# Kernel optimization log

Measured on AMD Instinct MI355X. Metric: run time of the kernel, lower is better.

The kernel has to match this reference:

```python
import jax, jax.numpy as jnp
import numpy as np

B, L, C, H, W = 2, 16, 16, 64, 64


def setup_inputs() -> dict:
    key = jax.random.key(0)
    k1, k2 = jax.random.split(key)
    # flows scaled so cumulative normalized-coordinate flows mostly stay in [-1, 1]
    flows = jax.random.normal(k1, (B, L, 2, H, W), dtype=jnp.float32) * 0.05
    images = jax.random.normal(k2, (B, L, C, H, W), dtype=jnp.float32)
    return {"flows": flows, "images": images}


def _bilinear_sample(images, gx, gy):
    # images: [B, Lj, C, H, W]; gx, gy: [B, Li, Lj, H, W] normalized coords in [-1, 1]
    # Replicates torch.nn.functional.grid_sample(mode='bilinear',
    # padding_mode='zeros', align_corners=False).
    Bs, Lj, Cs, Hs, Ws = images.shape
    ix = ((gx + 1.0) * Ws - 1.0) * 0.5  # pixel x coord
    iy = ((gy + 1.0) * Hs - 1.0) * 0.5  # pixel y coord
    x0f = jnp.floor(ix)
    y0f = jnp.floor(iy)
    wx = ix - x0f  # weight toward x0+1 (differentiable w.r.t. flow)
    wy = iy - y0f
    x0 = x0f.astype(jnp.int32)
    y0 = y0f.astype(jnp.int32)
    img_flat = images.reshape(Bs, Lj, Cs, Hs * Ws)

    def gather(xi, yi):
        valid = (xi >= 0) & (xi < Ws) & (yi >= 0) & (yi < Hs)  # [B,Li,Lj,H,W]
        lin = jnp.clip(yi, 0, Hs - 1) * Ws + jnp.clip(xi, 0, Ws - 1)
        lin_t = jnp.transpose(lin, (0, 2, 1, 3, 4))  # [B,Lj,Li,H,W]
        # per (b, j): gather [C, HW] at indices [Li, H, W] -> [C, Li, H, W]
        v = jax.vmap(jax.vmap(lambda im, l: im[:, l]))(img_flat, lin_t)
        v = jnp.transpose(v, (0, 3, 1, 2, 4, 5))  # [B,Li,Lj,C,H,W]
        return v * valid[:, :, :, None, :, :].astype(v.dtype)

    v00 = gather(x0, y0)
    v01 = gather(x0 + 1, y0)
    v10 = gather(x0, y0 + 1)
    v11 = gather(x0 + 1, y0 + 1)
    wX = wx[:, :, :, None, :, :]
    wY = wy[:, :, :, None, :, :]
    return (v00 * (1.0 - wX) * (1.0 - wY) + v01 * wX * (1.0 - wY)
            + v10 * (1.0 - wX) * wY + v11 * wX * wY)


def reference(flows, images):
    Bs, Ls, _, Hs, Ws = flows.shape
    dt = flows.dtype
    cum = jnp.cumsum(flows, axis=1)  # [B,L,2,H,W]
    # rel[b, i, j] = cum[b, i] - cum[b, j]  -> [B,Li,Lj,2,H,W]
    rel = cum[:, :, None] - cum[:, None, :]
    # base sampling grid (pixel centers in normalized coords)
    gx_base = (jnp.arange(Ws, dtype=dt) + 0.5) * (2.0 / Ws) - 1.0  # [W]
    gy_base = (jnp.arange(Hs, dtype=dt) + 0.5) * (2.0 / Hs) - 1.0  # [H]
    gx = gx_base + rel[:, :, :, 0]              # [B,Li,Lj,H,W]
    gy = gy_base[:, None] + rel[:, :, :, 1]     # [B,Li,Lj,H,W]
    gx = jnp.remainder(gx + 1.0, 2.0) - 1.0     # wrap x into [-1, 1)
    warped = _bilinear_sample(images, gx, gy)   # [B,Li,Lj,C,H,W]
    mask = jnp.tril(jnp.ones((Ls, Ls), dtype=dt))
    # causal accumulate over source index j
    return jnp.einsum('bijchw,ij->bichw', warped, mask)
```

## Files before the change

kernel.cpp:

```cpp
#include <hip/hip_runtime.h>

#define BB 2
#define LL 16
#define CC 16
#define HH 64
#define WW 64
#define HWSZ (HH * WW)
#define NSEG 36

__device__ __constant__ int SEG_I[NSEG] = {
    1, 2, 3, 4,
    5, 5, 6, 6, 7, 7, 8, 8,
    9, 9, 9, 10, 10, 10, 11, 11, 11, 12, 12, 12,
    13, 13, 13, 13, 14, 14, 14, 14, 15, 15, 15, 15};
__device__ __constant__ int SEG_J0[NSEG] = {
    0, 0, 0, 0,
    0, 4, 0, 4, 0, 4, 0, 4,
    0, 4, 8, 0, 4, 8, 0, 4, 8, 0, 4, 8,
    0, 4, 8, 12, 0, 4, 8, 12, 0, 4, 8, 12};

__device__ __constant__ signed char NSEG_OF_I[LL] = {0,1,1,1,1,2,2,2,2,3,3,3,3,4,4,4};
__device__ __constant__ signed char SEG_OF_I[LL][4] = {
    {0,0,0,0},
    {0,0,0,0}, {1,0,0,0}, {2,0,0,0}, {3,0,0,0},
    {4,5,0,0}, {6,7,0,0}, {8,9,0,0}, {10,11,0,0},
    {12,13,14,0}, {15,16,17,0}, {18,19,20,0}, {21,22,23,0},
    {24,25,26,27}, {28,29,30,31}, {32,33,34,35}};

#define CUM2_FLOATS (BB * LL * HWSZ * 2)
#define QP_FLOATS   (BB * LL * CC * HWSZ)

__global__ __launch_bounds__(256) void gsp_prep(
    const float* __restrict__ flows,
    const float* __restrict__ images,
    float2* __restrict__ cum2,
    float4* __restrict__ nhwc)
{
    if (blockIdx.x < 32) {
        const int gid = blockIdx.x * 256 + threadIdx.x;
        const int b   = gid >> 12;
        const int pix = gid & (HWSZ - 1);
        const float* fb = flows + (size_t)b * LL * 2 * HWSZ + pix;
        float vx[LL], vy[LL];
        #pragma unroll
        for (int l = 0; l < LL; ++l) {
            vx[l] = fb[(size_t)l * 2 * HWSZ];
            vy[l] = fb[(size_t)l * 2 * HWSZ + HWSZ];
        }
        #pragma unroll
        for (int l = 1; l < LL; ++l) { vx[l] += vx[l - 1]; vy[l] += vy[l - 1]; }
        float2* cb = cum2 + (size_t)b * LL * HWSZ + pix;
        #pragma unroll
        for (int l = 0; l < LL; ++l) {
            float2 v; v.x = vx[l]; v.y = vy[l];
            cb[(size_t)l * HWSZ] = v;
        }
    } else {
        const int gid  = (blockIdx.x - 32) * 256 + threadIdx.x;
        const int quad = gid & 3;
        const int pix  = (gid >> 2) & (HWSZ - 1);
        const int bl   = gid >> 14;

        const float* src = images + (size_t)(bl * CC + quad * 4) * HWSZ + pix;
        float4 v;
        v.x = src[0 * HWSZ];
        v.y = src[1 * HWSZ];
        v.z = src[2 * HWSZ];
        v.w = src[3 * HWSZ];
        nhwc[((size_t)bl * HWSZ + pix) * 4 + quad] = v;
    }
}

__global__ __launch_bounds__(256) void gsp_pairs(
    const float2* __restrict__ cum2,
    const float4* __restrict__ nhwc,
    float4* __restrict__ partial)
{
    const int tile = blockIdx.x & 63;
    const int seg  = (blockIdx.x >> 6) % NSEG;
    const int b    = blockIdx.x / (64 * NSEG);

    const int i    = SEG_I[seg];
    const int j0   = SEG_J0[seg];
    const int jmax = i - 1;

    const int psub = threadIdx.x >> 2;
    const int quad = threadIdx.x & 3;
    const int pix  = tile * 64 + psub;
    const int h = pix >> 6;
    const int w = pix & (WW - 1);

    const float2* cum_b  = cum2 + (size_t)b * LL * HWSZ + pix;
    const float4* nhwc_b = nhwc + (size_t)b * LL * HWSZ * 4;

    const float gxb = (w + 0.5f) * (2.0f / WW) - 1.0f;
    const float gyb = (h + 0.5f) * (2.0f / HH) - 1.0f;

    const float2 ci = cum_b[(size_t)i * HWSZ];
    int    jj[4];
    float2 cj[4];
    #pragma unroll
    for (int k = 0; k < 4; ++k) {
        jj[k] = min(j0 + k, jmax);
        cj[k] = cum_b[(size_t)jj[k] * HWSZ];
    }

    int   off[16];
    float fxk[4], fyk[4];
    float m00[4], m01[4], m10[4], m11[4];
    #pragma unroll
    for (int k = 0; k < 4; ++k) {
        float gx = gxb + (ci.x - cj[k].x);
        float gy = gyb + (ci.y - cj[k].y);

        float tt = gx + 1.0f;
        tt = tt - floorf(tt * 0.5f) * 2.0f;
        gx = tt - 1.0f;

        const float ix = ((gx + 1.0f) * WW - 1.0f) * 0.5f;
        const float iy = ((gy + 1.0f) * HH - 1.0f) * 0.5f;
        const float x0f = floorf(ix);
        const float y0f = floorf(iy);
        fxk[k] = ix - x0f;
        fyk[k] = iy - y0f;
        const int x0 = (int)x0f;
        const int y0 = (int)y0f;
        const int x1 = x0 + 1;
        const int y1 = y0 + 1;

        const bool vx0 = (x0 >= 0) && (x0 < WW);
        const bool vx1 = (x1 >= 0) && (x1 < WW);
        const bool vy0 = (y0 >= 0) && (y0 < HH);
        const bool vy1 = (y1 >= 0) && (y1 < HH);
        const float wpad = (j0 + k <= jmax) ? 1.0f : 0.0f;
        m00[k] = (vx0 && vy0) ? wpad : 0.0f;
        m01[k] = (vx1 && vy0) ? wpad : 0.0f;
        m10[k] = (vx0 && vy1) ? wpad : 0.0f;
        m11[k] = (vx1 && vy1) ? wpad : 0.0f;

        const int cx0 = min(max(x0, 0), WW - 1);
        const int cx1 = min(max(x1, 0), WW - 1);
        const int cy0 = min(max(y0, 0), HH - 1);
        const int cy1 = min(max(y1, 0), HH - 1);

        const int jbase = jj[k] * (HWSZ * 4) + quad;
        off[k * 4 + 0] = jbase + (cy0 * WW + cx0) * 4;
        off[k * 4 + 1] = jbase + (cy0 * WW + cx1) * 4;
        off[k * 4 + 2] = jbase + (cy1 * WW + cx0) * 4;
        off[k * 4 + 3] = jbase + (cy1 * WW + cx1) * 4;
    }

    float4 v[16];
    #pragma unroll
    for (int m = 0; m < 16; ++m) v[m] = nhwc_b[off[m]];

    float wgt[16];
    #pragma unroll
    for (int k = 0; k < 4; ++k) {
        const float fx = fxk[k], fy = fyk[k];
        wgt[k * 4 + 0] = m00[k] * (1.0f - fx) * (1.0f - fy);
        wgt[k * 4 + 1] = m01[k] * fx * (1.0f - fy);
        wgt[k * 4 + 2] = m10[k] * (1.0f - fx) * fy;
        wgt[k * 4 + 3] = m11[k] * fx * fy;
    }

    float4 s; s.x = 0.0f; s.y = 0.0f; s.z = 0.0f; s.w = 0.0f;
    #pragma unroll
    for (int m = 0; m < 16; ++m) {
        s.x += wgt[m] * v[m].x;
        s.y += wgt[m] * v[m].y;
        s.z += wgt[m] * v[m].z;
        s.w += wgt[m] * v[m].w;
    }
    partial[((size_t)(b * NSEG + seg) * HWSZ + pix) * 4 + quad] = s;
}

__global__ __launch_bounds__(256) void gsp_reduce(
    const float4* __restrict__ nhwc,
    const float4* __restrict__ partial,
    float* __restrict__ out)
{
    const int gid  = blockIdx.x * 256 + threadIdx.x;
    const int quad = gid & 3;
    const int pix  = (gid >> 2) & (HWSZ - 1);
    const int bl   = gid >> 14;
    const int b    = bl >> 4;
    const int i    = bl & 15;

    float4 s = nhwc[((size_t)bl * HWSZ + pix) * 4 + quad];

    const int n = NSEG_OF_I[i];
    for (int k = 0; k < n; ++k) {
        const int seg = SEG_OF_I[i][k];
        const float4 p = partial[((size_t)(b * NSEG + seg) * HWSZ + pix) * 4 + quad];
        s.x += p.x; s.y += p.y; s.z += p.z; s.w += p.w;
    }

    float* op = out + ((size_t)bl * CC + quad * 4) * HWSZ + pix;
    op[0 * HWSZ] = s.x;
    op[1 * HWSZ] = s.y;
    op[2 * HWSZ] = s.z;
    op[3 * HWSZ] = s.w;
}

extern "C" void kernel_launch(void* const* d_in, const int* in_sizes, int n_in,
                              void* d_out, int out_size, void* d_ws, size_t ws_size,
                              hipStream_t stream) {
    const float* flows  = (const float*)d_in[0];
    const float* images = (const float*)d_in[1];
    float* out = (float*)d_out;
    float2* cum2    = (float2*)d_ws;
    float*  nhwc    = (float*)d_ws + CUM2_FLOATS;
    float4* partial = (float4*)((float*)d_ws + CUM2_FLOATS + QP_FLOATS);

    gsp_prep<<<32 + 2048, 256, 0, stream>>>(flows, images, cum2, (float4*)nhwc);

    const int grid = BB * NSEG * 64;
    gsp_pairs<<<grid, 256, 0, stream>>>(cum2, (const float4*)nhwc, partial);

    gsp_reduce<<<2048, 256, 0, stream>>>((const float4*)nhwc, partial, out);
}
```

Baseline: 89.89 us.

## Store channel-last image copy in fp16 and widen per-thread channel group

The prep kernel now converts images to a packed half-precision channel-last buffer with 8 channels per 16-byte load. Each thread in the pair kernel gathers and accumulates 8 channels instead of 4, which halves the grid and the gather bytes. The reduce kernel reads the identity term directly from the fp32 input, so the fp32 copy is no longer used. This is meant to cut gather bandwidth and the number of transactions in the main kernel. It adds fp16 rounding error to the warped values, which may break tolerance.

New measurement: 85.97 us. -4.4%, faster.

```diff
diff --git a/kernel.cpp b/kernel.cpp
--- a/kernel.cpp
+++ b/kernel.cpp
@@ -1,4 +1,5 @@
 #include <hip/hip_runtime.h>
+#include <hip/hip_fp16.h>
 
 #define BB 2
 #define LL 16
@@ -28,13 +29,18 @@
     {24,25,26,27}, {28,29,30,31}, {32,33,34,35}};
 
 #define CUM2_FLOATS (BB * LL * HWSZ * 2)
-#define QP_FLOATS   (BB * LL * CC * HWSZ)
+#define H16_FLOATS  (BB * LL * HWSZ * 8)
+
+__device__ __forceinline__ float2 cvt2(unsigned int u) {
+    __half2 h = *reinterpret_cast<const __half2*>(&u);
+    return __half22float2(h);
+}
 
 __global__ __launch_bounds__(256) void gsp_prep(
     const float* __restrict__ flows,
     const float* __restrict__ images,
     float2* __restrict__ cum2,
-    float4* __restrict__ nhwc)
+    uint4* __restrict__ h16)
 {
     if (blockIdx.x < 32) {
         const int gid = blockIdx.x * 256 + threadIdx.x;
@@ -57,41 +63,47 @@
         }
     } else {
         const int gid  = (blockIdx.x - 32) * 256 + threadIdx.x;
-        const int quad = gid & 3;
-        const int pix  = (gid >> 2) & (HWSZ - 1);
-        const int bl   = gid >> 14;
-
-        const float* src = images + (size_t)(bl * CC + quad * 4) * HWSZ + pix;
-        float4 v;
-        v.x = src[0 * HWSZ];
-        v.y = src[1 * HWSZ];
-        v.z = src[2 * HWSZ];
-        v.w = src[3 * HWSZ];
-        nhwc[((size_t)bl * HWSZ + pix) * 4 + quad] = v;
+        const int half = gid & 1;
+        const int pix  = (gid >> 1) & (HWSZ - 1);
+        const int bl   = gid >> 13;
+
+        const float* src = images + (size_t)(bl * CC + half * 8) * HWSZ + pix;
+        unsigned short hs[8];
+        #pragma unroll
+        for (int m = 0; m < 8; ++m) {
+            __half h = __float2half(src[(size_t)m * HWSZ]);
+            hs[m] = *reinterpret_cast<unsigned short*>(&h);
+        }
+        uint4 v;
+        v.x = (unsigned)hs[0] | ((unsigned)hs[1] << 16);
+        v.y = (unsigned)hs[2] | ((unsigned)hs[3] << 16);
+        v.z = (unsigned)hs[4] | ((unsigned)hs[5] << 16);
+        v.w = (unsigned)hs[6] | ((unsigned)hs[7] << 16);
+        h16[((size_t)bl * HWSZ + pix) * 2 + half] = v;
     }
 }
 
 __global__ __launch_bounds__(256) void gsp_pairs(
     const float2* __restrict__ cum2,
-    const float4* __restrict__ nhwc,
+    const uint4* __restrict__ h16,
     float4* __restrict__ partial)
 {
-    const int tile = blockIdx.x & 63;
-    const int seg  = (blockIdx.x >> 6) % NSEG;
-    const int b    = blockIdx.x / (64 * NSEG);
+    const int tile = blockIdx.x & 31;
+    const int seg  = (blockIdx.x >> 5) % NSEG;
+    const int b    = blockIdx.x / (32 * NSEG);
 
     const int i    = SEG_I[seg];
     const int j0   = SEG_J0[seg];
     const int jmax = i - 1;
 
-    const int psub = threadIdx.x >> 2;
-    const int quad = threadIdx.x & 3;
-    const int pix  = tile * 64 + psub;
+    const int half = threadIdx.x & 1;
+    const int psub = threadIdx.x >> 1;
+    const int pix  = tile * 128 + psub;
     const int h = pix >> 6;
     const int w = pix & (WW - 1);
 
-    const float2* cum_b  = cum2 + (size_t)b * LL * HWSZ + pix;
-    const float4* nhwc_b = nhwc + (size_t)b * LL * HWSZ * 4;
+    const float2* cum_b = cum2 + (size_t)b * LL * HWSZ + pix;
+    const uint4*  h16_b = h16 + (size_t)b * LL * HWSZ * 2;
 
     const float gxb = (w + 0.5f) * (2.0f / WW) - 1.0f;
     const float gyb = (h + 0.5f) * (2.0f / HH) - 1.0f;
@@ -143,16 +155,16 @@
         const int cy0 = min(max(y0, 0), HH - 1);
         const int cy1 = min(max(y1, 0), HH - 1);
 
-        const int jbase = jj[k] * (HWSZ * 4) + quad;
-        off[k * 4 + 0] = jbase + (cy0 * WW + cx0) * 4;
-        off[k * 4 + 1] = jbase + (cy0 * WW + cx1) * 4;
-        off[k * 4 + 2] = jbase + (cy1 * WW + cx0) * 4;
-        off[k * 4 + 3] = jbase + (cy1 * WW + cx1) * 4;
-    }
-
-    float4 v[16];
-    #pragma unroll
-    for (int m = 0; m < 16; ++m) v[m] = nhwc_b[off[m]];
+        const int jbase = jj[k] * (HWSZ * 2) + half;
+        off[k * 4 + 0] = jbase + (cy0 * WW + cx0) * 2;
+        off[k * 4 + 1] = jbase + (cy0 * WW + cx1) * 2;
+        off[k * 4 + 2] = jbase + (cy1 * WW + cx0) * 2;
+        off[k * 4 + 3] = jbase + (cy1 * WW + cx1) * 2;
+    }
+
+    uint4 v[16];
+    #pragma unroll
+    for (int m = 0; m < 16; ++m) v[m] = h16_b[off[m]];
 
     float wgt[16];
     #pragma unroll
@@ -164,19 +176,30 @@
         wgt[k * 4 + 3] = m11[k] * fx * fy;
     }
 
-    float4 s; s.x = 0.0f; s.y = 0.0f; s.z = 0.0f; s.w = 0.0f;
+    float a0 = 0.f, a1 = 0.f, a2 = 0.f, a3 = 0.f;
+    float a4 = 0.f, a5 = 0.f, a6 = 0.f, a7 = 0.f;
     #pragma unroll
     for (int m = 0; m < 16; ++m) {
-        s.x += wgt[m] * v[m].x;
-        s.y += wgt[m] * v[m].y;
-        s.z += wgt[m] * v[m].z;
-        s.w += wgt[m] * v[m].w;
-    }
-    partial[((size_t)(b * NSEG + seg) * HWSZ + pix) * 4 + quad] = s;
+        const float wm = wgt[m];
+        const float2 p0 = cvt2(v[m].x);
+        const float2 p1 = cvt2(v[m].y);
+        const float2 p2 = cvt2(v[m].z);
+        const float2 p3 = cvt2(v[m].w);
+        a0 += wm * p0.x;  a1 += wm * p0.y;
+        a2 += wm * p1.x;  a3 += wm * p1.y;
+        a4 += wm * p2.x;  a5 += wm * p2.y;
+        a6 += wm * p3.x;  a7 += wm * p3.y;
+    }
+
+    float4* pp = partial + ((size_t)(b * NSEG + seg) * HWSZ + pix) * 4 + half * 2;
+    float4 s0; s0.x = a0; s0.y = a1; s0.z = a2; s0.w = a3;
+    float4 s1; s1.x = a4; s1.y = a5; s1.z = a6; s1.w = a7;
+    pp[0] = s0;
+    pp[1] = s1;
 }
 
 __global__ __launch_bounds__(256) void gsp_reduce(
-    const float4* __restrict__ nhwc,
+    const float* __restrict__ images,
     const float4* __restrict__ partial,
     float* __restrict__ out)
 {
@@ -187,7 +210,12 @@
     const int b    = bl >> 4;
     const int i    = bl & 15;
 
-    float4 s = nhwc[((size_t)bl * HWSZ + pix) * 4 + quad];
+    const float* ip = images + (size_t)(bl * CC + quad * 4) * HWSZ + pix;
+    float4 s;
+    s.x = ip[0 * HWSZ];
+    s.y = ip[1 * HWSZ];
+    s.z = ip[2 * HWSZ];
+    s.w = ip[3 * HWSZ];
 
     const int n = NSEG_OF_I[i];
     for (int k = 0; k < n; ++k) {
@@ -210,13 +238,13 @@
     const float* images = (const float*)d_in[1];
     float* out = (float*)d_out;
     float2* cum2    = (float2*)d_ws;
-    float*  nhwc    = (float*)d_ws + CUM2_FLOATS;
-    float4* partial = (float4*)((float*)d_ws + CUM2_FLOATS + QP_FLOATS);
-
-    gsp_prep<<<32 + 2048, 256, 0, stream>>>(flows, images, cum2, (float4*)nhwc);
-
-    const int grid = BB * NSEG * 64;
-    gsp_pairs<<<grid, 256, 0, stream>>>(cum2, (const float4*)nhwc, partial);
-
-    gsp_reduce<<<2048, 256, 0, stream>>>((const float4*)nhwc, partial, out);
-}
+    uint4*  h16     = (uint4*)((float*)d_ws + CUM2_FLOATS);
+    float4* partial = (float4*)((float*)d_ws + CUM2_FLOATS + H16_FLOATS);
+
+    gsp_prep<<<32 + 1024, 256, 0, stream>>>(flows, images, cum2, h16);
+
+    const int grid = BB * NSEG * 32;
+    gsp_pairs<<<grid, 256, 0, stream>>>(cum2, h16, partial);
+
+    gsp_reduce<<<2048, 256, 0, stream>>>(images, partial, out);
+}
```
